# Optimization experiments

Measured on AMD Instinct MI355X. Metric: run time of the kernel, lower is better.

## Reference

```python
import jax, jax.numpy as jnp
import numpy as np

N = 8192
IN_F = 512
OUT_F = 512
ALPHA = 0.2
NEG_BIG = -9.0e15


def setup_inputs() -> dict:
    key = jax.random.key(0)
    k1, k2, k3, k4 = jax.random.split(key, 4)
    adjacency = jax.random.randint(k1, (N, N), 0, 2, dtype=jnp.int32)
    features = jax.random.normal(k2, (N, IN_F), dtype=jnp.float32)
    # Linear weight stored as [in, out] (h = x @ W)
    W = jax.random.normal(k3, (IN_F, OUT_F), dtype=jnp.float32) * (1.0 / np.sqrt(IN_F))
    attn = jax.random.normal(k4, (2 * OUT_F, 1), dtype=jnp.float32) * 0.05
    return {"adjacency": adjacency, "features": features, "W": W, "attn": attn}


def reference(adjacency, features, W, attn):
    h = features @ W  # [N, F]
    # Additive decomposition of concat([h_i, h_j]) @ attn:
    # score_ij = a1 . h_i + a2 . h_j  (identical math, no NxNx2F tensor)
    a1 = attn[:OUT_F, 0]  # [F]
    a2 = attn[OUT_F:, 0]  # [F]
    s1 = h @ a1  # [N] contribution of source node i
    s2 = h @ a2  # [N] contribution of target node j
    e = jax.nn.leaky_relu(s1[:, None] + s2[None, :], negative_slope=ALPHA)  # [N, N]
    e = jnp.where(adjacency > 0, e, NEG_BIG)
    attention = jax.nn.softmax(e, axis=1)  # [N, N]
    h_prime = attention @ h  # [N, F]
    return jax.nn.elu(h_prime)
```

## Files before the change

### kernel.cpp

```cpp
#include <hip/hip_runtime.h>
#include <hip/hip_bf16.h>
#include <cstdint>

#define NN 8192
#define F 512
#define LOG2E 1.4426950408889634f

typedef __attribute__((ext_vector_type(8))) short bf16x8;
typedef __attribute__((ext_vector_type(4))) float f32x4;
typedef unsigned int uint32;
typedef unsigned long long u64;
typedef unsigned char uchar;

__device__ __forceinline__ short f2bf(float x){
  __hip_bfloat16 h = __float2bfloat16(x);
  return *reinterpret_cast<short*>(&h);
}

__global__ __launch_bounds__(256) void k_wa(const float* __restrict__ W, const float* __restrict__ attn,
                     float* __restrict__ wa){
  const int lane = threadIdx.x&63, wid = threadIdx.x>>6;
  const int id = blockIdx.x*4 + wid;
  const int b = id>>9, c = id&511;
  const float4* Wr = (const float4*)(W + (size_t)c*F);
  const float4* av = (const float4*)(attn + b*F);
  float s = 0.f;
  #pragma unroll
  for (int h=0;h<2;++h){
    const int k = lane + h*64;
    const float4 wv = Wr[k], a = av[k];
    s += wv.x*a.x + wv.y*a.y + wv.z*a.z + wv.w*a.w;
  }
  for (int off=32;off;off>>=1) s += __shfl_down(s,off);
  if (lane==0) wa[id] = s;
}

__global__ __launch_bounds__(256) void k_tw(const float* __restrict__ W, short* __restrict__ WbT){
  __shared__ short t[64][72];
  const int k0 = blockIdx.x*64, n0 = blockIdx.y*64;
  #pragma unroll
  for (int it=0;it<16;++it){
    const int idx = it*256 + threadIdx.x;
    const int r = idx>>6, c = idx&63;
    t[r][c] = f2bf(W[(size_t)(k0+r)*F + n0 + c]);
  }
  __syncthreads();
  #pragma unroll
  for (int it=0;it<2;++it){
    const int idx = it*256 + threadIdx.x;
    const int n = idx>>3, g = idx&7;
    short v[8];
    #pragma unroll
    for (int e=0;e<8;++e) v[e] = t[g*8+e][n];
    *(uint4*)(WbT + (size_t)(n0+n)*F + k0 + g*8) = *(const uint4*)v;
  }
}

__global__ __launch_bounds__(256) void k_prep(const float* __restrict__ X, const float* __restrict__ wa,
    short* __restrict__ Xb, float2* __restrict__ rowAB, uint32* __restrict__ uwb){
  const int lane = threadIdx.x&63, wid = threadIdx.x>>6;
  const int row = blockIdx.x*4 + wid;
  const float4* X4 = (const float4*)(X + (size_t)row*F);
  const float4* A4 = (const float4*)wa;
  const float4* B4 = (const float4*)(wa + F);
  uint2* Xb4 = (uint2*)(Xb + (size_t)row*F);
  float a1 = 0.f, a2 = 0.f;
  #pragma unroll
  for (int h=0;h<2;++h){
    const int c = lane + h*64;
    const float4 x = X4[c];
    const float4 a = A4[c];
    const float4 b = B4[c];
    a1 += x.x*a.x + x.y*a.y + x.z*a.z + x.w*a.w;
    a2 += x.x*b.x + x.y*b.y + x.z*b.z + x.w*b.w;
    short o[4] = {f2bf(x.x),f2bf(x.y),f2bf(x.z),f2bf(x.w)};
    Xb4[c] = *(const uint2*)o;
  }
  for (int off=32;off;off>>=1){ a1 += __shfl_down(a1,off); a2 += __shfl_down(a2,off); }
  if (lane==0){
    const float s1 = a1*LOG2E, s2 = a2*LOG2E;
    rowAB[row] = make_float2(exp2f(s1), exp2f(0.2f*s1));
    const float u = exp2f(s2), w = exp2f(0.2f*s2);
    uwb[row] = (uint32)(unsigned short)f2bf(u) | ((uint32)(unsigned short)f2bf(w)<<16);
  }
}

__global__ __launch_bounds__(256,2) void k_gemm1(const short* __restrict__ Xb,
    const short* __restrict__ WbT, short* __restrict__ HT){
  __shared__ char smem[33280];
  short* At = (short*)smem;
  short* Bt = (short*)(smem + 16384);
  const int tid=threadIdx.x, lane=tid&63, wid=tid>>6;
  const int m0 = blockIdx.x*128, n0 = blockIdx.y*128;
  f32x4 acc[2][8];
  #pragma unroll
  for (int a=0;a<2;++a)
    #pragma unroll
    for (int b=0;b<8;++b) acc[a][b] = (f32x4){0.f,0.f,0.f,0.f};

  for (int t=0;t<8;++t){
    const int k0 = t*64;
    __syncthreads();
    #pragma unroll
    for (int rnd=0;rnd<4;++rnd){
      const int s = rnd*256 + tid;
      const int n = s>>3, kc = s&7;
      uint4 va = *(const uint4*)(Xb  + (size_t)(m0+n)*F + k0 + kc*8);
      uint4 vb = *(const uint4*)(WbT + (size_t)(n0+n)*F + k0 + kc*8);
      const int off = n*128 + ((kc^(n&7))*16);
      *(uint4*)((char*)At + off) = va;
      *(uint4*)((char*)Bt + off) = vb;
    }
    __syncthreads();
    #pragma unroll
    for (int ks=0;ks<2;++ks){
      const int kc = ks*4 + (lane>>4);
      int r0 = wid*32 + (lane&15);
      int r1 = r0 + 16;
      bf16x8 af0 = *(const bf16x8*)((char*)At + r0*128 + ((kc^(r0&7))*16));
      bf16x8 af1 = *(const bf16x8*)((char*)At + r1*128 + ((kc^(r1&7))*16));
      #pragma unroll
      for (int nf=0;nf<8;++nf){
        const int c = nf*16 + (lane&15);
        bf16x8 bf = *(const bf16x8*)((char*)Bt + c*128 + ((kc^(c&7))*16));
        acc[0][nf] = __builtin_amdgcn_mfma_f32_16x16x32_bf16(af0, bf, acc[0][nf],0,0,0);
        acc[1][nf] = __builtin_amdgcn_mfma_f32_16x16x32_bf16(af1, bf, acc[1][nf],0,0,0);
      }
    }
  }
  __syncthreads();
  short* ct = (short*)smem;
  #pragma unroll
  for (int mf=0;mf<2;++mf)
    #pragma unroll
    for (int nf=0;nf<8;++nf)
      #pragma unroll
      for (int q=0;q<4;++q){
        int r = wid*32 + mf*16 + (lane>>4)*4 + q;
        int c = nf*16 + (lane&15);
        ct[r*130+c] = f2bf(acc[mf][nf][q]);
      }
  __syncthreads();
  {
    const int c = tid>>1, ih0 = (tid&1)*64;
    #pragma unroll
    for (int i8=0;i8<8;++i8){
      short v[8];
      #pragma unroll
      for (int e=0;e<8;++e) v[e] = ct[(ih0+i8*8+e)*130 + c];
      *(uint4*)(HT + (size_t)(n0+c)*NN + m0 + ih0 + i8*8) = *(const uint4*)v;
    }
  }
}

__global__ __launch_bounds__(256,2) void k_pv(const int* __restrict__ adj,
    const short* __restrict__ HT, const uint32* __restrict__ uwb,
    const float2* __restrict__ rowAB, float* __restrict__ Zp,
    float* __restrict__ P0, float* __restrict__ P1,
    float* __restrict__ P2, float* __restrict__ P3, int ksteps, int KS){
  __shared__ short Bt[512*64];
  __shared__ short At[64*64];
  __shared__ uint32 uwl[2048];
  const int tid=threadIdx.x, lane=tid&63, wid=tid>>6;
  int mx, kz;
  if (KS == 4){
    const int id = blockIdx.x;
    kz = (id&7)>>1;
    mx = ((id>>3)<<1) + (id&1);
  } else { kz = 0; mx = blockIdx.x; }
  const int m0 = mx*64;
  const int kz0 = kz*(ksteps*64);
  float* const outs[4] = {P0,P1,P2,P3};
  float* outP = outs[kz];

  {
    const uint4* src = (const uint4*)(uwb + kz0);
    uint4 v0 = src[tid], v1 = src[256+tid];
    ((uint4*)uwl)[tid] = v0; ((uint4*)uwl)[256+tid] = v1;
  }

  const int kcs = (tid&7) ^ ((tid>>3)&7);
  const short* gBa = HT + (size_t)(tid>>3)*NN + kz0 + kcs*8;

  const int ar = tid>>2, aq = tid&3;
  const float2 E = rowAB[m0 + ar];
  const float A0 = E.x, B0c = E.y;
  const int* adjp = adj + (size_t)(m0+ar)*NN + kz0 + aq*8;
  const int aoff0 = ar*128 + (((aq  ) ^ (ar&7))*16);
  const int aoff1 = ar*128 + (((aq+4) ^ (ar&7))*16);

  f32x4 acc[4][8];
  #pragma unroll
  for (int i=0;i<4;++i)
    #pragma unroll
    for (int j=0;j<8;++j) acc[i][j] = (f32x4){0.f,0.f,0.f,0.f};
  float zacc = 0.f;

  uint4 b0,b1,b2,b3,b4,b5,b6,b7;
  uint4 c0,c1,c2,c3,c4,c5,c6,c7;
  int4  aA0,aA1, aB0,aB1;

#define PV_BLOAD_H0(tt) { \
    const short* g = gBa + (size_t)(tt)*64; \
    b0 = *(const uint4*)(g);                   b1 = *(const uint4*)(g + (size_t)1*32*NN); \
    b2 = *(const uint4*)(g + (size_t)2*32*NN); b3 = *(const uint4*)(g + (size_t)3*32*NN); \
    b4 = *(const uint4*)(g + (size_t)4*32*NN); b5 = *(const uint4*)(g + (size_t)5*32*NN); \
    b6 = *(const uint4*)(g + (size_t)6*32*NN); b7 = *(const uint4*)(g + (size_t)7*32*NN); }

#define PV_BLOAD_H1(tt) { \
    const short* g = gBa + (size_t)256*NN + (size_t)(tt)*64; \
    c0 = *(const uint4*)(g);                   c1 = *(const uint4*)(g + (size_t)1*32*NN); \
    c2 = *(const uint4*)(g + (size_t)2*32*NN); c3 = *(const uint4*)(g + (size_t)3*32*NN); \
    c4 = *(const uint4*)(g + (size_t)4*32*NN); c5 = *(const uint4*)(g + (size_t)5*32*NN); \
    c6 = *(const uint4*)(g + (size_t)6*32*NN); c7 = *(const uint4*)(g + (size_t)7*32*NN); }

#define PV_BWRITE_H0() { \
    uint4* d = (uint4*)Bt; \
    d[      tid] = b0; d[ 256+tid] = b1; d[ 512+tid] = b2; d[ 768+tid] = b3; \
    d[1024+tid] = b4; d[1280+tid] = b5; d[1536+tid] = b6; d[1792+tid] = b7; }

#define PV_BWRITE_H1() { \
    uint4* d = (uint4*)Bt + 2048; \
    d[      tid] = c0; d[ 256+tid] = c1; d[ 512+tid] = c2; d[ 768+tid] = c3; \
    d[1024+tid] = c4; d[1280+tid] = c5; d[1536+tid] = c6; d[1792+tid] = c7; }

#define PV_ALOAD(r0v,r1v,h,tt) { \
    r0v = *(const int4*)(adjp + (size_t)(tt)*64 + (h)*32); \
    r1v = *(const int4*)(adjp + (size_t)(tt)*64 + (h)*32 + 4); }

#define PV_AGEN(aoffv, r0v, r1v, h, tt) { \
    const uint32* uwt = &uwl[(tt)*64 + (h)*32 + aq*8]; \
    const uint4 u0 = *(const uint4*)uwt; \
    const uint4 u1 = *(const uint4*)(uwt+4); \
    const uint32 pk[8] = {u0.x,u0.y,u0.z,u0.w,u1.x,u1.y,u1.z,u1.w}; \
    const int    aa[8] = {r0v.x,r0v.y,r0v.z,r0v.w,r1v.x,r1v.y,r1v.z,r1v.w}; \
    short av[8]; \
    _Pragma("unroll") \
    for (int e=0;e<8;++e){ \
      const float u = __uint_as_float(pk[e]<<16); \
      const float w = __uint_as_float(pk[e]&0xffff0000u); \
      float v = fmaxf(A0*u, B0c*w); \
      v = (aa[e] > 0) ? v : 0.f; \
      zacc += v; \
      av[e] = f2bf(v); } \
    *(uint4*)((char*)At + (aoffv)) = *(const uint4*)av; }

#define PV_MFMA64() { \
    _Pragma("unroll") \
    for (int ks=0;ks<2;++ks){ \
      const int kc = ks*4 + (lane>>4); \
      bf16x8 af[4]; \
      _Pragma("unroll") \
      for (int mf=0;mf<4;++mf){ \
        const int r = mf*16 + (lane&15); \
        af[mf] = *(const bf16x8*)((char*)At + r*128 + ((kc^(r&7))*16)); } \
      _Pragma("unroll") \
      for (int nf=0;nf<8;++nf){ \
        const int c = wid*128 + nf*16 + (lane&15); \
        const bf16x8 bv = *(const bf16x8*)((char*)Bt + c*128 + ((kc^(c&7))*16)); \
        _Pragma("unroll") \
        for (int mf=0;mf<4;++mf) \
          acc[mf][nf] = __builtin_amdgcn_mfma_f32_16x16x32_bf16(af[mf], bv, acc[mf][nf],0,0,0); } } }

  PV_ALOAD(aA0,aA1, 0, 0);
  PV_ALOAD(aB0,aB1, 1, 0);
  PV_BLOAD_H0(0);
  PV_BLOAD_H1(0);
  __syncthreads();
  PV_BWRITE_H0();
  PV_AGEN(aoff0, aA0,aA1, 0, 0);
  PV_BWRITE_H1();
  PV_AGEN(aoff1, aB0,aB1, 1, 0);
  __syncthreads();

  for (int t=0; t<ksteps; ++t){
    if (t+1 < ksteps){
      PV_BLOAD_H0(t+1);
      PV_BLOAD_H1(t+1);
      PV_ALOAD(aA0,aA1, 0, t+1);
      PV_ALOAD(aB0,aB1, 1, t+1);
    }
    PV_MFMA64();
    __syncthreads();
    if (t+1 < ksteps){
      PV_BWRITE_H0();
      PV_AGEN(aoff0, aA0,aA1, 0, t+1);
      PV_BWRITE_H1();
      PV_AGEN(aoff1, aB0,aB1, 1, t+1);
      __syncthreads();
    }
  }

  zacc += __shfl_xor(zacc, 1);
  zacc += __shfl_xor(zacc, 2);
  if (aq == 0) Zp[(size_t)kz*NN + m0 + ar] = zacc;
  #pragma unroll
  for (int mf=0;mf<4;++mf)
    #pragma unroll
    for (int nf=0;nf<8;++nf){
      const int col = wid*128 + nf*16 + (lane&15);
      #pragma unroll
      for (int qq=0;qq<4;++qq){
        const int row = m0 + mf*16 + (lane>>4)*4 + qq;
        outP[(size_t)row*F + col] = acc[mf][nf][qq];
      }
    }
#undef PV_BLOAD_H0
#undef PV_BLOAD_H1
#undef PV_BWRITE_H0
#undef PV_BWRITE_H1
#undef PV_ALOAD
#undef PV_AGEN
#undef PV_MFMA64
}

__global__ __launch_bounds__(256) void k_red(const float* __restrict__ P1,
    const float* __restrict__ P2, const float* __restrict__ P3,
    const float* __restrict__ Zp, float* __restrict__ out, int ks){
  const size_t i = ((size_t)blockIdx.x*256 + threadIdx.x)*4;
  const int row = (int)(i >> 9);
  float4 a = *(float4*)(out+i);
  float Z = Zp[row];
  if (ks > 1){
    Z += Zp[NN+row] + Zp[2*NN+row] + Zp[3*NN+row];
    const float4 b1 = *(const float4*)(P1+i);
    const float4 b2 = *(const float4*)(P2+i);
    const float4 b3 = *(const float4*)(P3+i);
    a.x += b1.x+b2.x+b3.x; a.y += b1.y+b2.y+b3.y;
    a.z += b1.z+b2.z+b3.z; a.w += b1.w+b2.w+b3.w;
  }
  const float s = 1.f/Z;
  a.x*=s; a.y*=s; a.z*=s; a.w*=s;
  a.x = (a.x>0.f)?a.x:expm1f(a.x);
  a.y = (a.y>0.f)?a.y:expm1f(a.y);
  a.z = (a.z>0.f)?a.z:expm1f(a.z);
  a.w = (a.w>0.f)?a.w:expm1f(a.w);
  *(float4*)(out+i) = a;
}

extern "C" void kernel_launch(void* const* d_in, const int* in_sizes, int n_in,
                              void* d_out, int out_size, void* d_ws, size_t ws_size,
                              hipStream_t stream) {
  (void)in_sizes; (void)n_in; (void)out_size;
  const int*   adj  = (const int*)d_in[0];
  const float* X    = (const float*)d_in[1];
  const float* W    = (const float*)d_in[2];
  const float* attn = (const float*)d_in[3];
  float* out = (float*)d_out;
  char* ws = (char*)d_ws;
  short*  HT   = (short*)(ws);
  short*  Xb   = (short*)(ws + 8388608);
  short*  WbT  = (short*)(ws + 16777216);
  uint32* uwb  = (uint32*)(ws + 17301504);
  float2* rowAB= (float2*)(ws + 17334272);
  float*  wa   = (float*)(ws + 17399808);
  float*  Zp   = (float*)(ws + 17403904);
  float*  P1   = (float*)(ws + 17534976);
  float*  P2   = (float*)(ws + 34312192);
  float*  P3   = (float*)(ws + 51089408);
  const int KS = (ws_size >= 67866624ull) ? 4 : 1;
  const int ksteps = 128/KS;

  k_wa   <<<dim3(256),    dim3(256), 0, stream>>>(W, attn, wa);
  k_tw   <<<dim3(8,8),    dim3(256), 0, stream>>>(W, WbT);
  k_prep <<<dim3(2048),   dim3(256), 0, stream>>>(X, wa, Xb, rowAB, uwb);
  k_gemm1<<<dim3(64,4),   dim3(256), 0, stream>>>(Xb, WbT, HT);
  k_pv   <<<dim3(128*KS), dim3(256), 0, stream>>>(adj, HT, uwb, rowAB, Zp, out, P1, P2, P3, ksteps, KS);
  k_red  <<<dim3(4096),   dim3(256), 0, stream>>>(P1, P2, P3, Zp, out, KS);
}
```

Measured before the change: 147.6 us.

## Double-buffer attention A tile and generate it before the barrier, reading weights from global

The P·V kernel now keeps two A-tile buffers in shared memory, so the attention values for the next k-step are computed and written before the barrier instead of after it. This overlaps the exp/mask/convert work with the tail of the current MFMA phase and shortens the serialized section between the two barriers. The per-column weight table is no longer staged into LDS and is read straight from global (cached) memory, which frees LDS and removes the initial staging. The cost is extra global loads inside the inner loop and more live registers at the point where A generation overlaps the MFMAs.

```diff
diff --git a/kernel.cpp b/kernel.cpp
--- a/kernel.cpp
+++ b/kernel.cpp
@@ -159,8 +159,7 @@
     float* __restrict__ P0, float* __restrict__ P1,
     float* __restrict__ P2, float* __restrict__ P3, int ksteps, int KS){
   __shared__ short Bt[512*64];
-  __shared__ short At[64*64];
-  __shared__ uint32 uwl[2048];
+  __shared__ short At2[2][64*64];
   const int tid=threadIdx.x, lane=tid&63, wid=tid>>6;
   int mx, kz;
   if (KS == 4){
@@ -173,12 +172,6 @@
   float* const outs[4] = {P0,P1,P2,P3};
   float* outP = outs[kz];
 
-  {
-    const uint4* src = (const uint4*)(uwb + kz0);
-    uint4 v0 = src[tid], v1 = src[256+tid];
-    ((uint4*)uwl)[tid] = v0; ((uint4*)uwl)[256+tid] = v1;
-  }
-
   const int kcs = (tid&7) ^ ((tid>>3)&7);
   const short* gBa = HT + (size_t)(tid>>3)*NN + kz0 + kcs*8;
 
@@ -186,6 +179,7 @@
   const float2 E = rowAB[m0 + ar];
   const float A0 = E.x, B0c = E.y;
   const int* adjp = adj + (size_t)(m0+ar)*NN + kz0 + aq*8;
+  const uint32* uwp = uwb + kz0 + aq*8;
   const int aoff0 = ar*128 + (((aq  ) ^ (ar&7))*16);
   const int aoff1 = ar*128 + (((aq+4) ^ (ar&7))*16);
 
@@ -228,8 +222,8 @@
     r0v = *(const int4*)(adjp + (size_t)(tt)*64 + (h)*32); \
     r1v = *(const int4*)(adjp + (size_t)(tt)*64 + (h)*32 + 4); }
 
-#define PV_AGEN(aoffv, r0v, r1v, h, tt) { \
-    const uint32* uwt = &uwl[(tt)*64 + (h)*32 + aq*8]; \
+#define PV_AGEN(buf, aoffv, r0v, r1v, h, tt) { \
+    const uint32* uwt = uwp + (size_t)(tt)*64 + (h)*32; \
     const uint4 u0 = *(const uint4*)uwt; \
     const uint4 u1 = *(const uint4*)(uwt+4); \
     const uint32 pk[8] = {u0.x,u0.y,u0.z,u0.w,u1.x,u1.y,u1.z,u1.w}; \
@@ -243,9 +237,9 @@
       v = (aa[e] > 0) ? v : 0.f; \
       zacc += v; \
       av[e] = f2bf(v); } \
-    *(uint4*)((char*)At + (aoffv)) = *(const uint4*)av; }
-
-#define PV_MFMA64() { \
+    *(uint4*)((char*)(At2[buf]) + (aoffv)) = *(const uint4*)av; }
+
+#define PV_MFMA64(buf) { \
     _Pragma("unroll") \
     for (int ks=0;ks<2;++ks){ \
       const int kc = ks*4 + (lane>>4); \
@@ -253,7 +247,7 @@
       _Pragma("unroll") \
       for (int mf=0;mf<4;++mf){ \
         const int r = mf*16 + (lane&15); \
-        af[mf] = *(const bf16x8*)((char*)At + r*128 + ((kc^(r&7))*16)); } \
+        af[mf] = *(const bf16x8*)((char*)(At2[buf]) + r*128 + ((kc^(r&7))*16)); } \
       _Pragma("unroll") \
       for (int nf=0;nf<8;++nf){ \
         const int c = wid*128 + nf*16 + (lane&15); \
@@ -266,11 +260,10 @@
   PV_ALOAD(aB0,aB1, 1, 0);
   PV_BLOAD_H0(0);
   PV_BLOAD_H1(0);
-  __syncthreads();
+  PV_AGEN(0, aoff0, aA0,aA1, 0, 0);
+  PV_AGEN(0, aoff1, aB0,aB1, 1, 0);
   PV_BWRITE_H0();
-  PV_AGEN(aoff0, aA0,aA1, 0, 0);
   PV_BWRITE_H1();
-  PV_AGEN(aoff1, aB0,aB1, 1, 0);
   __syncthreads();
 
   for (int t=0; t<ksteps; ++t){
@@ -280,13 +273,15 @@
       PV_ALOAD(aA0,aA1, 0, t+1);
       PV_ALOAD(aB0,aB1, 1, t+1);
     }
-    PV_MFMA64();
+    PV_MFMA64(t&1);
+    if (t+1 < ksteps){
+      PV_AGEN((t+1)&1, aoff0, aA0,aA1, 0, t+1);
+      PV_AGEN((t+1)&1, aoff1, aB0,aB1, 1, t+1);
+    }
     __syncthreads();
     if (t+1 < ksteps){
       PV_BWRITE_H0();
-      PV_AGEN(aoff0, aA0,aA1, 0, t+1);
       PV_BWRITE_H1();
-      PV_AGEN(aoff1, aB0,aB1, 1, t+1);
       __syncthreads();
     }
   }
```

Measured after the change: 166.2 us. 12.6% more time.
